# Optimization experiments

Measured on AMD Instinct MI355X. Metric: run time of the kernel, lower is better.

## Reference

```python
import jax, jax.numpy as jnp
import numpy as np

DEPTH = 8
DIM = 1024
DI = 2 * DIM        # d_inner (expand=2)
DSTATE = 16         # d_state
DCONV = 4           # conv kernel width
DTRANK = DIM // 16  # dt_rank = ceil(d_model/16) = 64
B = 2
L = 2048
EPS = 1e-5


def setup_inputs() -> dict:
    key = jax.random.key(0)
    ks = jax.random.split(key, 8)
    s = 0.02
    A_log = jnp.broadcast_to(
        jnp.log(jnp.arange(1, DSTATE + 1, dtype=jnp.float32)), (DEPTH, DI, DSTATE)
    )
    return {
        "x": jax.random.normal(ks[0], (B, L, DIM), jnp.float32),
        "in_proj_w": jax.random.normal(ks[1], (DEPTH, 2 * DI, DIM), jnp.float32) * s,
        "conv_w": jax.random.normal(ks[2], (DEPTH, DI, DCONV), jnp.float32) * s,
        "conv_b": jnp.zeros((DEPTH, DI), jnp.float32),
        "x_proj_w": jax.random.normal(ks[3], (DEPTH, DTRANK + 2 * DSTATE, DI), jnp.float32) * s,
        "dt_proj_w": jax.random.normal(ks[4], (DEPTH, DI, DTRANK), jnp.float32) * s,
        "dt_proj_b": jax.random.normal(ks[5], (DEPTH, DI), jnp.float32) * 0.1,
        "A_log": A_log + 0.0,
        "D": jnp.ones((DEPTH, DI), jnp.float32),
        "out_proj_w": jax.random.normal(ks[6], (DEPTH, DIM, DI), jnp.float32) * s,
        "rms_w": jnp.ones((DEPTH, DIM), jnp.float32),
    }


def _selective_scan(xs, delta, Bm, Cm, A):
    # xs, delta: [B, L, DI]; Bm, Cm: [B, L, DSTATE]; A: [DI, DSTATE]
    def step(h, t):
        dt, Bt, Ct, xt = t  # [B,DI], [B,N], [B,N], [B,DI]
        dA = jnp.exp(dt[:, :, None] * A)                      # [B,DI,N]
        h = dA * h + (dt * xt)[:, :, None] * Bt[:, None, :]   # [B,DI,N]
        y = jnp.einsum('bdn,bn->bd', h, Ct)                   # [B,DI]
        return h, y

    h0 = jnp.zeros((xs.shape[0], xs.shape[2], A.shape[1]), xs.dtype)
    ts = (delta.transpose(1, 0, 2), Bm.transpose(1, 0, 2),
          Cm.transpose(1, 0, 2), xs.transpose(1, 0, 2))
    _, ys = jax.lax.scan(step, h0, ts)  # ys: [L,B,DI]
    return ys.transpose(1, 0, 2)


def _mamba(x, Wi, cw, cb, Wx, Wdt, bdt, A_log, Dp, Wo):
    # in_proj (no bias): [B,L,DIM] -> [B,L,2*DI]
    xz = jnp.einsum('bld,ed->ble', x, Wi)
    xs, z = jnp.split(xz, 2, axis=-1)
    # depthwise causal conv1d, kernel DCONV, left pad DCONV-1
    xc = jax.lax.conv_general_dilated(
        xs.transpose(0, 2, 1), cw[:, None, :], (1,), [(DCONV - 1, 0)],
        dimension_numbers=('NCH', 'OIH', 'NCH'), feature_group_count=DI)
    xs = jax.nn.silu(xc + cb[None, :, None]).transpose(0, 2, 1)  # [B,L,DI]
    # x_proj -> dt, B, C
    xdbl = jnp.einsum('bld,ed->ble', xs, Wx)
    dt, Bm, Cm = jnp.split(xdbl, [DTRANK, DTRANK + DSTATE], axis=-1)
    delta = jax.nn.softplus(jnp.einsum('blr,dr->bld', dt, Wdt) + bdt)  # [B,L,DI]
    A = -jnp.exp(A_log)  # [DI, DSTATE]
    y = _selective_scan(xs, delta, Bm, Cm, A) + xs * Dp
    y = y * jax.nn.silu(z)
    return jnp.einsum('bld,ed->ble', y, Wo)  # out_proj, no bias


def _rmsnorm(x, w):
    return x * jax.lax.rsqrt(jnp.mean(x * x, axis=-1, keepdims=True) + EPS) * w


def reference(x, in_proj_w, conv_w, conv_b, x_proj_w, dt_proj_w, dt_proj_b,
              A_log, D, out_proj_w, rms_w):
    for i in range(DEPTH):
        x = _mamba(x, in_proj_w[i], conv_w[i], conv_b[i], x_proj_w[i],
                   dt_proj_w[i], dt_proj_b[i], A_log[i], D[i], out_proj_w[i])
        x = _rmsnorm(x, rms_w[i])
    return x
```

## Files before the change

kernel.cpp:

```cpp
#include <hip/hip_runtime.h>
#include <cstddef>

#define DEPTH  8
#define DIMM   1024
#define DI     2048
#define NST    16
#define DCONVK 4
#define DTRANK 64
#define BB     2
#define LL     2048
#define MM     (BB*LL)
#define BD     (BB*DI)
#define CHK    32
#define LC     (LL/CHK)
#define LOG2E  1.44269504088896f

typedef __attribute__((ext_vector_type(8))) short bf16x8;
typedef __attribute__((ext_vector_type(4))) float f32x4;

__device__ __forceinline__ unsigned short f2bf(float f) {
  unsigned int u = __float_as_uint(f);
  unsigned int r = (u + 0x7fffu + ((u >> 16) & 1u)) >> 16;
  return (unsigned short)r;
}
__device__ __forceinline__ float bf2f(unsigned short h) {
  return __uint_as_float(((unsigned int)h) << 16);
}

__global__ __launch_bounds__(256) void cvt2_k(const float* __restrict__ x,
                                              unsigned short* __restrict__ p,
                                              size_t n) {
  size_t i = ((size_t)blockIdx.x * 256 + threadIdx.x) * 4;
  float4 v = *(const float4*)(x + i);
  float vv[4] = {v.x, v.y, v.z, v.w};
  unsigned short u1[4], u2[4];
#pragma unroll
  for (int k = 0; k < 4; ++k) {
    unsigned short h1 = f2bf(vv[k]);
    u1[k] = h1;
    u2[k] = f2bf(vv[k] - bf2f(h1));
  }
  *(ushort4*)(p + i)     = make_ushort4(u1[0], u1[1], u1[2], u1[3]);
  *(ushort4*)(p + n + i) = make_ushort4(u2[0], u2[1], u2[2], u2[3]);
}

template <int BN, int NSPLIT>
__global__ __launch_bounds__(512, 2) void gemm2ph(
    const unsigned short* __restrict__ Ap, int lda_a, int pstr_a,
    const unsigned short* __restrict__ Bp, int lda_b, int pstr_b,
    float* __restrict__ C0, float* __restrict__ C1, int N, int Ktot) {
  constexpr int BM  = 256;
  constexpr int BF  = BN / 64;
  constexpr int BL  = BN / 128;
  constexpr int RA1 = BM * 32;
  constexpr int RB0 = 2 * BM * 32;
  constexpr int RB1 = 2 * BM * 32 + BN * 32;
  constexpr int BUFS = (2 * BM + 2 * BN) * 32;
  __shared__ unsigned short S[2 * BUFS];

  const int t  = threadIdx.x;
  const int w  = t >> 6;
  const int l  = t & 63;
  const int lm = l & 15;
  const int qs = ((l >> 4) << 3) ^ (((lm >> 1) & 3) << 3);

  const int nx   = gridDim.x;
  const int nwg  = nx * gridDim.y;
  const int flat = blockIdx.y * nx + blockIdx.x;
  const int swz  = (flat & 7) * (nwg >> 3) + (flat >> 3);
  const int m0 = (swz / nx) * BM;
  const int n0 = (swz % nx) * BN;
  const int z  = (NSPLIT == 2) ? blockIdx.z : 0;
  const int KS = Ktot / NSPLIT;

  const int wm = (w & 1) << 7;
  const int wn = (w >> 1) * (BN / 4);

  const int rr = t >> 2;
  const int kq = ((t & 3) ^ ((rr >> 1) & 3)) << 3;
  const unsigned short* srcA = Ap + (size_t)(m0 + rr) * lda_a + (size_t)z * KS + kq;
  const unsigned short* srcB = Bp + (size_t)(n0 + rr) * lda_b + (size_t)z * KS + kq;
  const size_t a128 = (size_t)128 * lda_a;
  const size_t b128 = (size_t)128 * lda_b;
  const int dbase = (w << 6) * 8;

#define GI(p_, off_)                                                           \
  __builtin_amdgcn_global_load_lds(                                            \
      (const __attribute__((address_space(1))) unsigned int*)(p_),             \
      (__attribute__((address_space(3))) unsigned int*)&S[bnext + (off_) + dbase], \
      16, 0, 0)

#define GI_PH0(kb_)                                                            \
  { GI(srcA + (kb_), 0); GI(srcA + a128 + (kb_), 4096);                        \
    GI(srcB + (kb_), RB0);                                                     \
    if (BL == 2) GI(srcB + b128 + (kb_), RB0 + 4096);                          \
    GI(srcB + (size_t)pstr_b + (kb_), RB1);                                    \
    if (BL == 2) GI(srcB + (size_t)pstr_b + b128 + (kb_), RB1 + 4096); }

#define GI_PH1(kb_)                                                            \
  { GI(srcA + (size_t)pstr_a + (kb_), RA1);                                    \
    GI(srcA + (size_t)pstr_a + a128 + (kb_), RA1 + 4096); }

  f32x4 acc[8][BF];
#pragma unroll
  for (int i = 0; i < 8; ++i)
#pragma unroll
    for (int j = 0; j < BF; ++j) acc[i][j] = (f32x4){0.f, 0.f, 0.f, 0.f};

  {
    const int bnext = 0;
    GI_PH0((size_t)0);
    GI_PH1((size_t)0);
  }
  asm volatile("s_waitcnt vmcnt(2)" ::: "memory");
  __builtin_amdgcn_s_barrier();

  const int NT = KS >> 5;
#pragma unroll 2
  for (int ti = 0; ti < NT; ++ti) {
    const int bcur  = (ti & 1) ? BUFS : 0;
    const int bnext = (ti & 1) ? 0 : BUFS;
    const size_t kb = (size_t)((ti + 1 < NT) ? (ti + 1) : 0) * 32;
    const unsigned short* Sb = &S[bcur];
    bf16x8 a[8], b0[BF], b1[BF];

#pragma unroll
    for (int i = 0; i < 8; ++i)
      a[i] = *(const bf16x8*)&Sb[(wm + i * 16 + lm) * 32 + qs];
#pragma unroll
    for (int j = 0; j < BF; ++j)
      b0[j] = *(const bf16x8*)&Sb[RB0 + (wn + j * 16 + lm) * 32 + qs];
#pragma unroll
    for (int j = 0; j < BF; ++j)
      b1[j] = *(const bf16x8*)&Sb[RB1 + (wn + j * 16 + lm) * 32 + qs];
    GI_PH0(kb);
    if constexpr (BN == 256) asm volatile("s_waitcnt vmcnt(6)" ::: "memory");
    else                     asm volatile("s_waitcnt vmcnt(4)" ::: "memory");
    __builtin_amdgcn_s_barrier();
    asm volatile("s_waitcnt lgkmcnt(0)" ::: "memory");
    __builtin_amdgcn_s_setprio(1);
#pragma unroll
    for (int i = 0; i < 8; ++i)
#pragma unroll
      for (int j = 0; j < BF; ++j)
        acc[i][j] = __builtin_amdgcn_mfma_f32_16x16x32_bf16(a[i], b0[j], acc[i][j], 0, 0, 0);
#pragma unroll
    for (int i = 0; i < 8; ++i)
#pragma unroll
      for (int j = 0; j < BF; ++j)
        acc[i][j] = __builtin_amdgcn_mfma_f32_16x16x32_bf16(a[i], b1[j], acc[i][j], 0, 0, 0);
    __builtin_amdgcn_s_setprio(0);
    __builtin_amdgcn_s_barrier();

#pragma unroll
    for (int i = 0; i < 8; ++i)
      a[i] = *(const bf16x8*)&Sb[RA1 + (wm + i * 16 + lm) * 32 + qs];
    GI_PH1(kb);
    asm volatile("s_waitcnt vmcnt(2)" ::: "memory");
    __builtin_amdgcn_s_barrier();
    asm volatile("s_waitcnt lgkmcnt(0)" ::: "memory");
    __builtin_amdgcn_s_setprio(1);
#pragma unroll
    for (int i = 0; i < 8; ++i)
#pragma unroll
      for (int j = 0; j < BF; ++j)
        acc[i][j] = __builtin_amdgcn_mfma_f32_16x16x32_bf16(a[i], b0[j], acc[i][j], 0, 0, 0);
    __builtin_amdgcn_s_setprio(0);
    __builtin_amdgcn_s_barrier();
  }
#undef GI_PH1
#undef GI_PH0
#undef GI

  float* Cc = (NSPLIT == 2 && blockIdx.z) ? C1 : C0;
  const int row0 = (l >> 4) << 2;
#pragma unroll
  for (int i = 0; i < 8; ++i)
#pragma unroll
    for (int j = 0; j < BF; ++j)
#pragma unroll
      for (int r = 0; r < 4; ++r) {
        int m = m0 + wm + i * 16 + row0 + r;
        int n = n0 + wn + j * 16 + lm;
        Cc[(size_t)m * N + n] = acc[i][j][r];
      }
}

__global__ __launch_bounds__(256) void dtproj_mp(const unsigned short* __restrict__ Ap,
                                                 const unsigned short* __restrict__ Bp,
                                                 const float* __restrict__ bdt,
                                                 float* __restrict__ Cd) {
  __shared__ unsigned short S[32768];
  const int t  = threadIdx.x;
  const int w  = t >> 6;
  const int l  = t & 63;
  const int lm = l & 15;
  const int q8 = (l >> 4) << 3;
  const int qs = q8 ^ (((lm >> 1) & 3) << 3);
  const int m0 = blockIdx.y * 128;
  const int n0 = blockIdx.x * 128;
  const int wm = (w & 1) << 6;
  const int wn = (w >> 1) << 6;

#pragma unroll
  for (int it = 0; it < 16; ++it) {
    int c  = it * 256 + t;
    int kt = c >> 11;
    int c2 = c & 2047;
    const unsigned short* base;
    int r, aslot;
    if (c2 < 1024) {
      int p = c2 >> 9; int wi = c2 & 511; r = wi >> 2; aslot = wi & 3;
      base = Ap + (size_t)p * (MM * 64) + (size_t)(m0 + r) * 64;
    } else {
      int c3 = c2 - 1024;
      int p = c3 >> 9; int wi = c3 & 511; r = wi >> 2; aslot = wi & 3;
      base = Bp + (size_t)p * (DI * 64) + (size_t)(n0 + r) * 64;
    }
    int kq = (aslot ^ ((r >> 1) & 3)) << 3;
    __builtin_amdgcn_global_load_lds(
        (const __attribute__((address_space(1))) unsigned int*)(base + kt * 32 + kq),
        (__attribute__((address_space(3))) unsigned int*)&S[(size_t)(it * 256 + (w << 6)) * 8],
        16, 0, 0);
  }
  __syncthreads();

  f32x4 acc[4][4];
#pragma unroll
  for (int i = 0; i < 4; ++i)
#pragma unroll
    for (int j = 0; j < 4; ++j) acc[i][j] = (f32x4){0.f, 0.f, 0.f, 0.f};

#pragma unroll
  for (int kt = 0; kt < 2; ++kt) {
    const int RA = kt * 16384;
    const int RB = kt * 16384 + 8192;
    bf16x8 a0[4], aX[4], b0[4];
#pragma unroll
    for (int i = 0; i < 4; ++i)
      a0[i] = *(const bf16x8*)&S[RA + (wm + i * 16 + lm) * 32 + qs];
#pragma unroll
    for (int j = 0; j < 4; ++j)
      b0[j] = *(const bf16x8*)&S[RB + (wn + j * 16 + lm) * 32 + qs];
#pragma unroll
    for (int i = 0; i < 4; ++i)
#pragma unroll
      for (int j = 0; j < 4; ++j)
        acc[i][j] = __builtin_amdgcn_mfma_f32_16x16x32_bf16(a0[i], b0[j], acc[i][j], 0, 0, 0);
#pragma unroll
    for (int j = 0; j < 4; ++j)
      aX[j] = *(const bf16x8*)&S[RB + 4096 + (wn + j * 16 + lm) * 32 + qs];
#pragma unroll
    for (int i = 0; i < 4; ++i)
#pragma unroll
      for (int j = 0; j < 4; ++j)
        acc[i][j] = __builtin_amdgcn_mfma_f32_16x16x32_bf16(a0[i], aX[j], acc[i][j], 0, 0, 0);
#pragma unroll
    for (int i = 0; i < 4; ++i)
      aX[i] = *(const bf16x8*)&S[RA + 4096 + (wm + i * 16 + lm) * 32 + qs];
#pragma unroll
    for (int i = 0; i < 4; ++i)
#pragma unroll
      for (int j = 0; j < 4; ++j)
        acc[i][j] = __builtin_amdgcn_mfma_f32_16x16x32_bf16(aX[i], b0[j], acc[i][j], 0, 0, 0);
  }

  const int row0 = (l >> 4) << 2;
#pragma unroll
  for (int j = 0; j < 4; ++j) {
    int n = n0 + wn + j * 16 + lm;
    float bv = bdt[n];
#pragma unroll
    for (int i = 0; i < 4; ++i)
#pragma unroll
      for (int r = 0; r < 4; ++r) {
        int m = m0 + wm + i * 16 + row0 + r;
        float x = acc[i][j][r] + bv;
        Cd[(size_t)m * DI + n] = fmaxf(x, 0.f) + log1pf(expf(-fabsf(x)));
      }
  }
}

#define XPN 96
__global__ __launch_bounds__(256) void xproj_part_k(const float* __restrict__ A,
                                                    const float* __restrict__ W,
                                                    float* __restrict__ Cp) {
  __shared__ float As[16][128];
  __shared__ float Ws[16][XPN];
  const int t  = threadIdx.x;
  const int tx = t & 15;
  const int ty = t >> 4;
  const int m0 = blockIdx.x * 128;
  const int kb = blockIdx.y * 256;
  float acc[8][6];
#pragma unroll
  for (int i = 0; i < 8; ++i)
#pragma unroll
    for (int j = 0; j < 6; ++j) acc[i][j] = 0.f;

  for (int k0 = kb; k0 < kb + 256; k0 += 16) {
#pragma unroll
    for (int e = t; e < 512; e += 256) {
      int r = e >> 2, cq = (e & 3) << 2;
      float4 v = *(const float4*)(A + (size_t)(m0 + r) * DI + k0 + cq);
      As[cq+0][r] = v.x; As[cq+1][r] = v.y; As[cq+2][r] = v.z; As[cq+3][r] = v.w;
    }
    for (int e = t; e < 384; e += 256) {
      int r = e >> 2, cq = (e & 3) << 2;
      float4 v = *(const float4*)(W + (size_t)r * DI + k0 + cq);
      Ws[cq+0][r] = v.x; Ws[cq+1][r] = v.y; Ws[cq+2][r] = v.z; Ws[cq+3][r] = v.w;
    }
    __syncthreads();
#pragma unroll
    for (int kk = 0; kk < 16; ++kk) {
      float a[8], b[6];
#pragma unroll
      for (int i = 0; i < 8; ++i) a[i] = As[kk][ty*8 + i];
#pragma unroll
      for (int j = 0; j < 6; ++j) b[j] = Ws[kk][tx*6 + j];
#pragma unroll
      for (int i = 0; i < 8; ++i)
#pragma unroll
        for (int j = 0; j < 6; ++j) acc[i][j] += a[i] * b[j];
    }
    __syncthreads();
  }
  float* cp = Cp + (size_t)blockIdx.y * MM * XPN;
#pragma unroll
  for (int i = 0; i < 8; ++i)
#pragma unroll
    for (int j = 0; j < 6; ++j)
      cp[(size_t)(m0 + ty*8 + i) * XPN + tx*6 + j] = acc[i][j];
}

__global__ __launch_bounds__(256) void xproj_red_k(const float* __restrict__ Cp,
                                                   float* __restrict__ o,
                                                   unsigned short* __restrict__ dtp) {
  int i = blockIdx.x * 256 + threadIdx.x;
  float s = 0.f;
#pragma unroll
  for (int ks = 0; ks < 8; ++ks) s += Cp[(size_t)ks * (MM * XPN) + i];
  o[i] = s;
  int m = i / 96, col = i - m * 96;
  if (col < DTRANK) {
    unsigned short h1 = f2bf(s);
    dtp[(size_t)m * DTRANK + col] = h1;
    dtp[(size_t)MM * DTRANK + (size_t)m * DTRANK + col] = f2bf(s - bf2f(h1));
  }
}

__device__ __forceinline__ float fast_silu(float x) {
  return x * __builtin_amdgcn_rcpf(1.f + exp2f(-LOG2E * x));
}

__global__ __launch_bounds__(256) void conv_silu_k(const float* __restrict__ xz,
                                                   const float* __restrict__ cw,
                                                   const float* __restrict__ cb,
                                                   float* __restrict__ xc) {
  int idx = blockIdx.x * 256 + threadIdx.x;
  int c  = idx & (DI - 1);
  int bl = idx >> 11;
  int l  = bl & (LL - 1);
  float acc = cb[c];
#pragma unroll
  for (int k = 0; k < DCONVK; ++k) {
    int ls = l - (DCONVK - 1) + k;
    if (ls >= 0)
      acc += xz[(size_t)(bl - (DCONVK - 1) + k) * (2*DI) + c] * cw[c*DCONVK + k];
  }
  xc[idx] = fast_silu(acc);
}

__global__ __launch_bounds__(256) void scan_pass1(const float* __restrict__ delta,
                                                  const float* __restrict__ xc,
                                                  const float* __restrict__ xdbl,
                                                  const float* __restrict__ A_log,
                                                  float* __restrict__ Hc,
                                                  float* __restrict__ Sdt) {
  const int t  = threadIdx.x;
  const int c  = blockIdx.x >> 6;
  const int g  = blockIdx.x & 63;
  const int q  = t >> 2;
  const int nq = t & 3;
  const int ch = g * 64 + q;
  const int b  = ch >> 11;
  const int d  = ch & (DI - 1);
  const size_t rowbase = (size_t)b * LL + (size_t)c * LC;

  __shared__ float Bs[LC * 16];
  { int row = t >> 2, seg = t & 3;
    *(float4*)&Bs[row * 16 + seg * 4] =
        *(const float4*)(xdbl + (rowbase + row) * 96 + DTRANK + seg * 4);
  }
  __syncthreads();

  float4 al = *(const float4*)(A_log + (size_t)d * NST + nq * 4);
  const float Av0 = -expf(al.x) * LOG2E, Av1 = -expf(al.y) * LOG2E;
  const float Av2_ = -expf(al.z) * LOG2E, Av3 = -expf(al.w) * LOG2E;
  float h0 = 0.f, h1 = 0.f, h2 = 0.f, h3 = 0.f, S = 0.f;

#define P1_SU 4
  float aD[P1_SU], aX[P1_SU];
  float bD[P1_SU], bX[P1_SU];

#define P1_LOAD(l0, D_, X_)                                            \
  { _Pragma("unroll")                                                  \
    for (int u = 0; u < P1_SU; ++u) {                                  \
      size_t bl = rowbase + (l0) + u;                                  \
      D_[u] = delta[bl * DI + d];                                      \
      X_[u] = xc[bl * DI + d];                                         \
    } }

#define P1_COMP(l0, D_, X_)                                            \
  { _Pragma("unroll")                                                  \
    for (int u = 0; u < P1_SU; ++u) {                                  \
      float4 Bv = *(const float4*)&Bs[((l0) + u) * 16 + nq * 4];       \
      float dt = D_[u], uB = dt * X_[u];                               \
      h0 = fmaf(exp2f(dt * Av0), h0, uB * Bv.x);                       \
      h1 = fmaf(exp2f(dt * Av1), h1, uB * Bv.y);                       \
      h2 = fmaf(exp2f(dt * Av2_), h2, uB * Bv.z);                      \
      h3 = fmaf(exp2f(dt * Av3), h3, uB * Bv.w);                       \
      S += dt;                                                         \
    } }

  P1_LOAD(0, aD, aX);
  for (int l0 = 0; l0 < LC; l0 += 2 * P1_SU) {
    P1_LOAD(l0 + P1_SU, bD, bX);
    P1_COMP(l0, aD, aX);
    if (l0 + 2 * P1_SU < LC) P1_LOAD(l0 + 2 * P1_SU, aD, aX);
    P1_COMP(l0 + P1_SU, bD, bX);
  }
#undef P1_LOAD
#undef P1_COMP
  size_t hi = ((size_t)c * BD + ch) * NST + nq * 4;
  float4 hv; hv.x = h0; hv.y = h1; hv.z = h2; hv.w = h3;
  *(float4*)(Hc + hi) = hv;
  if (nq == 0) Sdt[(size_t)c * BD + ch] = S;
}

__global__ __launch_bounds__(256) void scan_pass2(float* __restrict__ Hc,
                                                  const float* __restrict__ Sdt,
                                                  const float* __restrict__ A_log) {
  const int g  = blockIdx.x * 256 + threadIdx.x;
  const int n  = g & (NST - 1);
  const int ch = g >> 4;
  const int d  = ch & (DI - 1);
  const float Av2 = -expf(A_log[d * NST + n]) * LOG2E;
  float Sv[CHK];
#pragma unroll
  for (int c = 0; c < CHK; ++c) Sv[c] = Sdt[(size_t)c * BD + ch];
  float h = 0.f;
  float tmp = Hc[(size_t)ch * NST + n];
#pragma unroll
  for (int c = 0; c < CHK; ++c) {
    size_t idx = ((size_t)c * BD + ch) * NST + n;
    float tnext = (c + 1 < CHK) ? Hc[((size_t)(c+1) * BD + ch) * NST + n] : 0.f;
    Hc[idx] = h;
    h = fmaf(exp2f(Av2 * Sv[c]), h, tmp);
    tmp = tnext;
  }
}

__global__ __launch_bounds__(256) void scan_pass3(const float* __restrict__ delta,
                                                  const float* __restrict__ xc,
                                                  const float* __restrict__ xdbl,
                                                  const float* __restrict__ A_log,
                                                  float* __restrict__ xzp,
                                                  const float* __restrict__ Dp,
                                                  const float* __restrict__ Hc) {
  const int t  = threadIdx.x;
  const int c  = blockIdx.x >> 6;
  const int g  = blockIdx.x & 63;
  const int q  = t >> 2;
  const int nq = t & 3;
  const int ch = g * 64 + q;
  const int b  = ch >> 11;
  const int d  = ch & (DI - 1);
  const size_t rowbase = (size_t)b * LL + (size_t)c * LC;

  __shared__ float BCs[LC * 32];
  {
#pragma unroll
    for (int e = t; e < 512; e += 256) {
      int row = e >> 3, seg = e & 7;
      *(float4*)&BCs[row * 32 + seg * 4] =
          *(const float4*)(xdbl + (rowbase + row) * 96 + DTRANK + seg * 4);
    }
  }
  __syncthreads();

  float4 al = *(const float4*)(A_log + (size_t)d * NST + nq * 4);
  const float Av0 = -expf(al.x) * LOG2E, Av1 = -expf(al.y) * LOG2E;
  const float Av2_ = -expf(al.z) * LOG2E, Av3 = -expf(al.w) * LOG2E;
  const float Dv = Dp[d];
  float4 hv = *(const float4*)(Hc + ((size_t)c * BD + ch) * NST + nq * 4);
  float h0 = hv.x, h1 = hv.y, h2 = hv.z, h3 = hv.w;
  unsigned short* yp = (unsigned short*)xzp;

#define P3_SU 2
  float aD[P3_SU], aX[P3_SU], aZ[P3_SU];
  float bD[P3_SU], bX[P3_SU], bZ[P3_SU];

#define P3_LOAD(l0, D_, X_, Z_)                                        \
  { _Pragma("unroll")                                                  \
    for (int u = 0; u < P3_SU; ++u) {                                  \
      size_t bl = rowbase + (l0) + u;                                  \
      D_[u] = delta[bl * DI + d];                                      \
      X_[u] = xc[bl * DI + d];                                         \
      Z_[u] = xzp[bl * (2*DI) + DI + d];                               \
    } }

#define P3_COMP(l0, D_, X_, Z_)                                        \
  { _Pragma("unroll")                                                  \
    for (int u = 0; u < P3_SU; ++u) {                                  \
      float4 Bv = *(const float4*)&BCs[((l0) + u) * 32 + nq * 4];      \
      float4 Cv = *(const float4*)&BCs[((l0) + u) * 32 + 16 + nq * 4]; \
      float dt = D_[u], uB = dt * X_[u];                               \
      h0 = fmaf(exp2f(dt * Av0), h0, uB * Bv.x);                       \
      h1 = fmaf(exp2f(dt * Av1), h1, uB * Bv.y);                       \
      h2 = fmaf(exp2f(dt * Av2_), h2, uB * Bv.z);                      \
      h3 = fmaf(exp2f(dt * Av3), h3, uB * Bv.w);                       \
      float s = fmaf(h1, Cv.y, h0 * Cv.x);                             \
      float t2 = fmaf(h3, Cv.w, h2 * Cv.z);                            \
      s += t2;                                                         \
      s += __shfl_xor(s, 1, 4);                                        \
      s += __shfl_xor(s, 2, 4);                                        \
      if (nq == 0) {                                                   \
        float yv = (s + X_[u] * Dv) * fast_silu(Z_[u]);                \
        unsigned short y1 = f2bf(yv);                                  \
        unsigned short y2 = f2bf(yv - bf2f(y1));                       \
        size_t bl = rowbase + (l0) + u;                                \
        yp[bl * 8192 + d] = y1;                                        \
        yp[bl * 8192 + 2048 + d] = y2;                                 \
      }                                                                \
    } }

  P3_LOAD(0, aD, aX, aZ);
  for (int l0 = 0; l0 < LC; l0 += 2 * P3_SU) {
    P3_LOAD(l0 + P3_SU, bD, bX, bZ);
    P3_COMP(l0, aD, aX, aZ);
    if (l0 + 2 * P3_SU < LC) P3_LOAD(l0 + 2 * P3_SU, aD, aX, aZ);
    P3_COMP(l0 + P3_SU, bD, bX, bZ);
  }
#undef P3_LOAD
#undef P3_COMP
}

template <bool PLANES>
__global__ __launch_bounds__(256) void rmsnorm_k(const float* __restrict__ x,
                                                 const float* __restrict__ x2,
                                                 const float* __restrict__ w,
                                                 float* __restrict__ o,
                                                 unsigned short* __restrict__ op) {
  int row = blockIdx.x;
  const float* xr  = x  + (size_t)row * DIMM;
  const float* x2r = x2 + (size_t)row * DIMM;
  float s = 0.f;
  for (int i = threadIdx.x; i < DIMM; i += 256) {
    float v = xr[i] + x2r[i]; s += v * v;
  }
#pragma unroll
  for (int off = 32; off > 0; off >>= 1) s += __shfl_xor(s, off, 64);
  __shared__ float red[4];
  if ((threadIdx.x & 63) == 0) red[threadIdx.x >> 6] = s;
  __syncthreads();
  float tot = red[0] + red[1] + red[2] + red[3];
  float scale = rsqrtf(tot * (1.0f / DIMM) + 1e-5f);
  for (int i = threadIdx.x; i < DIMM; i += 256) {
    float v = (xr[i] + x2r[i]) * scale * w[i];
    if (PLANES) {
      unsigned short h1 = f2bf(v);
      op[(size_t)row * DIMM + i] = h1;
      op[(size_t)MM * DIMM + (size_t)row * DIMM + i] = f2bf(v - bf2f(h1));
    } else {
      o[(size_t)row * DIMM + i] = v;
    }
  }
}

extern "C" void kernel_launch(void* const* d_in, const int* in_sizes, int n_in,
                              void* d_out, int out_size, void* d_ws, size_t ws_size,
                              hipStream_t stream) {
  (void)in_sizes; (void)n_in; (void)out_size; (void)ws_size;
  const float* x_in    = (const float*)d_in[0];
  const float* Wi_all  = (const float*)d_in[1];
  const float* cw_all  = (const float*)d_in[2];
  const float* cb_all  = (const float*)d_in[3];
  const float* Wx_all  = (const float*)d_in[4];
  const float* Wdt_all = (const float*)d_in[5];
  const float* bdt_all = (const float*)d_in[6];
  const float* Alog_all= (const float*)d_in[7];
  const float* D_all   = (const float*)d_in[8];
  const float* Wo_all  = (const float*)d_in[9];
  const float* rw_all  = (const float*)d_in[10];
  float* out = (float*)d_out;

  float* ws    = (float*)d_ws;
  float* xz    = ws;
  float* xc    = xz   + (size_t)MM * 2 * DI;
  float* xdbl  = xc   + (size_t)MM * DI;
  float* delta = xdbl + (size_t)MM * 96;
  float* xbuf  = delta+ (size_t)MM * DI;
  float* outtmp = xc;

  unsigned short* xpl  = (unsigned short*)delta;
  unsigned short* wipl = (unsigned short*)xc;
  unsigned short* wopl = (unsigned short*)(xc + (size_t)4194304);
  float*          Cp   = delta;
  float* part1 = delta + (size_t)4194304;
  float* Hc   = xbuf;
  float* Sdt  = Hc + (size_t)CHK * BD * NST;
  unsigned short* dtpl  = (unsigned short*)(xbuf + 2228224);
  unsigned short* wdtpl = (unsigned short*)(xbuf + 2490368);

  const int EW_GRID = (MM * DI) / 256;
  const int SCAN_GRID = CHK * 64;

  for (int i = 0; i < DEPTH; ++i) {
    const float* Wi   = Wi_all  + (size_t)i * (2*DI) * DIMM;
    const float* cw   = cw_all  + (size_t)i * DI * DCONVK;
    const float* cb   = cb_all  + (size_t)i * DI;
    const float* Wx   = Wx_all  + (size_t)i * 96 * DI;
    const float* Wdt  = Wdt_all + (size_t)i * DI * DTRANK;
    const float* bdt  = bdt_all + (size_t)i * DI;
    const float* Alog = Alog_all+ (size_t)i * DI * NST;
    const float* Dp   = D_all   + (size_t)i * DI;
    const float* Wo   = Wo_all  + (size_t)i * DIMM * DI;
    const float* rw   = rw_all  + (size_t)i * DIMM;

    if (i == 0)
      cvt2_k<<<(MM*DIMM)/1024, 256, 0, stream>>>(x_in, xpl, (size_t)MM * DIMM);
    cvt2_k<<<((2*DI)*DIMM)/1024, 256, 0, stream>>>(Wi, wipl, (size_t)(2*DI) * DIMM);
    gemm2ph<256,1><<<dim3((2*DI)/256, MM/256, 1), 512, 0, stream>>>(
        xpl, DIMM, MM*DIMM, wipl, DIMM, (2*DI)*DIMM, xz, nullptr, 2*DI, DIMM);
    conv_silu_k<<<EW_GRID, 256, 0, stream>>>(xz, cw, cb, xc);
    xproj_part_k<<<dim3(MM/128, 8), 256, 0, stream>>>(xc, Wx, Cp);
    xproj_red_k<<<(MM*XPN)/256, 256, 0, stream>>>(Cp, xdbl, dtpl);
    cvt2_k<<<(DI*DTRANK)/1024, 256, 0, stream>>>(Wdt, wdtpl, (size_t)DI * DTRANK);
    dtproj_mp<<<dim3(DI/128, MM/128), 256, 0, stream>>>(dtpl, wdtpl, bdt, delta);
    scan_pass1<<<SCAN_GRID, 256, 0, stream>>>(delta, xc, xdbl, Alog, Hc, Sdt);
    scan_pass2<<<(BD*NST)/256, 256, 0, stream>>>(Hc, Sdt, Alog);
    scan_pass3<<<SCAN_GRID, 256, 0, stream>>>(delta, xc, xdbl, Alog, xz, Dp, Hc);
    cvt2_k<<<(DIMM*DI)/1024, 256, 0, stream>>>(Wo, wopl, (size_t)DIMM * DI);
    gemm2ph<128,2><<<dim3(DIMM/128, MM/256, 2), 512, 0, stream>>>(
        (const unsigned short*)xz, 8192, 2048, wopl, DI, DIMM*DI,
        outtmp, part1, DIMM, DI);
    if (i < DEPTH - 1)
      rmsnorm_k<true><<<MM, 256, 0, stream>>>(outtmp, part1, rw, nullptr, xpl);
    else
      rmsnorm_k<false><<<MM, 256, 0, stream>>>(outtmp, part1, rw, out, nullptr);
  }
}
```

Measured before the change: 3.259 ms.

## Split GEMM K-step into three load phases and stage scan tiles in LDS

The split-precision GEMM now issues the B-low plane load as its own phase. Each K-step runs three MFMA phases (a0·b0, a0·b1, a1·b0), so the global-to-LDS copies interleave more finely with compute, and the vmcnt waits are adjusted to match. The scan pass1 and pass3 kernels now load delta, xc and z tiles into shared memory with coalesced float4 loads instead of strided per-thread scalar loads. Pass3 also buffers the bf16 output planes in LDS and writes them back vectorised. This adds barriers and LDS use, which may lower occupancy, and relies on correct vmcnt counts.

```diff
diff --git a/kernel.cpp b/kernel.cpp
--- a/kernel.cpp
+++ b/kernel.cpp
@@ -45,7 +45,7 @@
 }
 
 template <int BN, int NSPLIT>
-__global__ __launch_bounds__(512, 2) void gemm2ph(
+__global__ __launch_bounds__(512, 2) void gemm3ph(
     const unsigned short* __restrict__ Ap, int lda_a, int pstr_a,
     const unsigned short* __restrict__ Bp, int lda_b, int pstr_b,
     float* __restrict__ C0, float* __restrict__ C1, int N, int Ktot) {
@@ -54,7 +54,7 @@
   constexpr int BL  = BN / 128;
   constexpr int RA1 = BM * 32;
   constexpr int RB0 = 2 * BM * 32;
-  constexpr int RB1 = 2 * BM * 32 + BN * 32;
+  constexpr int RB1 = RB0 + BN * 32;
   constexpr int BUFS = (2 * BM + 2 * BN) * 32;
   __shared__ unsigned short S[2 * BUFS];
 
@@ -93,11 +93,13 @@
 #define GI_PH0(kb_)                                                            \
   { GI(srcA + (kb_), 0); GI(srcA + a128 + (kb_), 4096);                        \
     GI(srcB + (kb_), RB0);                                                     \
-    if (BL == 2) GI(srcB + b128 + (kb_), RB0 + 4096);                          \
-    GI(srcB + (size_t)pstr_b + (kb_), RB1);                                    \
-    if (BL == 2) GI(srcB + (size_t)pstr_b + b128 + (kb_), RB1 + 4096); }
+    if constexpr (BL == 2) GI(srcB + b128 + (kb_), RB0 + 4096); }
 
 #define GI_PH1(kb_)                                                            \
+  { GI(srcB + (size_t)pstr_b + (kb_), RB1);                                    \
+    if constexpr (BL == 2) GI(srcB + (size_t)pstr_b + b128 + (kb_), RB1 + 4096); }
+
+#define GI_PH2(kb_)                                                            \
   { GI(srcA + (size_t)pstr_a + (kb_), RA1);                                    \
     GI(srcA + (size_t)pstr_a + a128 + (kb_), RA1 + 4096); }
 
@@ -111,8 +113,10 @@
     const int bnext = 0;
     GI_PH0((size_t)0);
     GI_PH1((size_t)0);
-  }
-  asm volatile("s_waitcnt vmcnt(2)" ::: "memory");
+    GI_PH2((size_t)0);
+  }
+  if constexpr (BN == 256) asm volatile("s_waitcnt vmcnt(4)" ::: "memory");
+  else                     asm volatile("s_waitcnt vmcnt(3)" ::: "memory");
   __builtin_amdgcn_s_barrier();
 
   const int NT = KS >> 5;
@@ -130,10 +134,24 @@
 #pragma unroll
     for (int j = 0; j < BF; ++j)
       b0[j] = *(const bf16x8*)&Sb[RB0 + (wn + j * 16 + lm) * 32 + qs];
+    GI_PH0(kb);
+    if constexpr (BN == 256) asm volatile("s_waitcnt vmcnt(6)" ::: "memory");
+    else                     asm volatile("s_waitcnt vmcnt(5)" ::: "memory");
+    __builtin_amdgcn_s_barrier();
+    asm volatile("s_waitcnt lgkmcnt(0)" ::: "memory");
+    __builtin_amdgcn_s_setprio(1);
+#pragma unroll
+    for (int i = 0; i < 8; ++i)
+#pragma unroll
+      for (int j = 0; j < BF; ++j)
+        acc[i][j] = __builtin_amdgcn_mfma_f32_16x16x32_bf16(a[i], b0[j], acc[i][j], 0, 0, 0);
+    __builtin_amdgcn_s_setprio(0);
+    __builtin_amdgcn_s_barrier();
+
 #pragma unroll
     for (int j = 0; j < BF; ++j)
       b1[j] = *(const bf16x8*)&Sb[RB1 + (wn + j * 16 + lm) * 32 + qs];
-    GI_PH0(kb);
+    GI_PH1(kb);
     if constexpr (BN == 256) asm volatile("s_waitcnt vmcnt(6)" ::: "memory");
     else                     asm volatile("s_waitcnt vmcnt(4)" ::: "memory");
     __builtin_amdgcn_s_barrier();
@@ -143,11 +161,6 @@
     for (int i = 0; i < 8; ++i)
 #pragma unroll
       for (int j = 0; j < BF; ++j)
-        acc[i][j] = __builtin_amdgcn_mfma_f32_16x16x32_bf16(a[i], b0[j], acc[i][j], 0, 0, 0);
-#pragma unroll
-    for (int i = 0; i < 8; ++i)
-#pragma unroll
-      for (int j = 0; j < BF; ++j)
         acc[i][j] = __builtin_amdgcn_mfma_f32_16x16x32_bf16(a[i], b1[j], acc[i][j], 0, 0, 0);
     __builtin_amdgcn_s_setprio(0);
     __builtin_amdgcn_s_barrier();
@@ -155,8 +168,9 @@
 #pragma unroll
     for (int i = 0; i < 8; ++i)
       a[i] = *(const bf16x8*)&Sb[RA1 + (wm + i * 16 + lm) * 32 + qs];
-    GI_PH1(kb);
-    asm volatile("s_waitcnt vmcnt(2)" ::: "memory");
+    GI_PH2(kb);
+    if constexpr (BN == 256) asm volatile("s_waitcnt vmcnt(4)" ::: "memory");
+    else                     asm volatile("s_waitcnt vmcnt(3)" ::: "memory");
     __builtin_amdgcn_s_barrier();
     asm volatile("s_waitcnt lgkmcnt(0)" ::: "memory");
     __builtin_amdgcn_s_setprio(1);
@@ -168,6 +182,7 @@
     __builtin_amdgcn_s_setprio(0);
     __builtin_amdgcn_s_barrier();
   }
+#undef GI_PH2
 #undef GI_PH1
 #undef GI_PH0
 #undef GI
@@ -385,12 +400,22 @@
   const int ch = g * 64 + q;
   const int b  = ch >> 11;
   const int d  = ch & (DI - 1);
+  const int dbs = (g & 31) * 64;
   const size_t rowbase = (size_t)b * LL + (size_t)c * LC;
 
   __shared__ float Bs[LC * 16];
+  __shared__ float Ds[LC][64];
+  __shared__ float Xs[LC][64];
   { int row = t >> 2, seg = t & 3;
     *(float4*)&Bs[row * 16 + seg * 4] =
         *(const float4*)(xdbl + (rowbase + row) * 96 + DTRANK + seg * 4);
+  }
+#pragma unroll
+  for (int e = t; e < LC * 16; e += 256) {
+    int row = e >> 4, seg = (e & 15) << 2;
+    size_t ga = (rowbase + row) * DI + dbs + seg;
+    *(float4*)&Ds[row][seg] = *(const float4*)(delta + ga);
+    *(float4*)&Xs[row][seg] = *(const float4*)(xc + ga);
   }
   __syncthreads();
 
@@ -399,39 +424,18 @@
   const float Av2_ = -expf(al.z) * LOG2E, Av3 = -expf(al.w) * LOG2E;
   float h0 = 0.f, h1 = 0.f, h2 = 0.f, h3 = 0.f, S = 0.f;
 
-#define P1_SU 4
-  float aD[P1_SU], aX[P1_SU];
-  float bD[P1_SU], bX[P1_SU];
-
-#define P1_LOAD(l0, D_, X_)                                            \
-  { _Pragma("unroll")                                                  \
-    for (int u = 0; u < P1_SU; ++u) {                                  \
-      size_t bl = rowbase + (l0) + u;                                  \
-      D_[u] = delta[bl * DI + d];                                      \
-      X_[u] = xc[bl * DI + d];                                         \
-    } }
-
-#define P1_COMP(l0, D_, X_)                                            \
-  { _Pragma("unroll")                                                  \
-    for (int u = 0; u < P1_SU; ++u) {                                  \
-      float4 Bv = *(const float4*)&Bs[((l0) + u) * 16 + nq * 4];       \
-      float dt = D_[u], uB = dt * X_[u];                               \
-      h0 = fmaf(exp2f(dt * Av0), h0, uB * Bv.x);                       \
-      h1 = fmaf(exp2f(dt * Av1), h1, uB * Bv.y);                       \
-      h2 = fmaf(exp2f(dt * Av2_), h2, uB * Bv.z);                      \
-      h3 = fmaf(exp2f(dt * Av3), h3, uB * Bv.w);                       \
-      S += dt;                                                         \
-    } }
-
-  P1_LOAD(0, aD, aX);
-  for (int l0 = 0; l0 < LC; l0 += 2 * P1_SU) {
-    P1_LOAD(l0 + P1_SU, bD, bX);
-    P1_COMP(l0, aD, aX);
-    if (l0 + 2 * P1_SU < LC) P1_LOAD(l0 + 2 * P1_SU, aD, aX);
-    P1_COMP(l0 + P1_SU, bD, bX);
-  }
-#undef P1_LOAD
-#undef P1_COMP
+#pragma unroll 4
+  for (int l = 0; l < LC; ++l) {
+    float dt = Ds[l][q];
+    float xv = Xs[l][q];
+    float4 Bv = *(const float4*)&Bs[l * 16 + nq * 4];
+    float uB = dt * xv;
+    h0 = fmaf(exp2f(dt * Av0), h0, uB * Bv.x);
+    h1 = fmaf(exp2f(dt * Av1), h1, uB * Bv.y);
+    h2 = fmaf(exp2f(dt * Av2_), h2, uB * Bv.z);
+    h3 = fmaf(exp2f(dt * Av3), h3, uB * Bv.w);
+    S += dt;
+  }
   size_t hi = ((size_t)c * BD + ch) * NST + nq * 4;
   float4 hv; hv.x = h0; hv.y = h1; hv.z = h2; hv.w = h3;
   *(float4*)(Hc + hi) = hv;
@@ -476,16 +480,29 @@
   const int ch = g * 64 + q;
   const int b  = ch >> 11;
   const int d  = ch & (DI - 1);
+  const int dbs = (g & 31) * 64;
   const size_t rowbase = (size_t)b * LL + (size_t)c * LC;
 
   __shared__ float BCs[LC * 32];
-  {
-#pragma unroll
-    for (int e = t; e < 512; e += 256) {
-      int row = e >> 3, seg = e & 7;
-      *(float4*)&BCs[row * 32 + seg * 4] =
-          *(const float4*)(xdbl + (rowbase + row) * 96 + DTRANK + seg * 4);
-    }
+  __shared__ float Ds[LC][64];
+  __shared__ float Xs[LC][64];
+  __shared__ float Zs[LC][64];
+  __shared__ unsigned short Y1s[LC][64];
+  __shared__ unsigned short Y2s[LC][64];
+#pragma unroll
+  for (int e = t; e < 512; e += 256) {
+    int row = e >> 3, seg = e & 7;
+    *(float4*)&BCs[row * 32 + seg * 4] =
+        *(const float4*)(xdbl + (rowbase + row) * 96 + DTRANK + seg * 4);
+  }
+#pragma unroll
+  for (int e = t; e < LC * 16; e += 256) {
+    int row = e >> 4, seg = (e & 15) << 2;
+    size_t ga = (rowbase + row) * DI + dbs + seg;
+    *(float4*)&Ds[row][seg] = *(const float4*)(delta + ga);
+    *(float4*)&Xs[row][seg] = *(const float4*)(xc + ga);
+    *(float4*)&Zs[row][seg] =
+        *(const float4*)(xzp + (rowbase + row) * (2*DI) + DI + dbs + seg);
   }
   __syncthreads();
 
@@ -495,55 +512,40 @@
   const float Dv = Dp[d];
   float4 hv = *(const float4*)(Hc + ((size_t)c * BD + ch) * NST + nq * 4);
   float h0 = hv.x, h1 = hv.y, h2 = hv.z, h3 = hv.w;
+
+#pragma unroll 2
+  for (int l = 0; l < LC; ++l) {
+    float dt = Ds[l][q];
+    float xv = Xs[l][q];
+    float4 Bv = *(const float4*)&BCs[l * 32 + nq * 4];
+    float4 Cv = *(const float4*)&BCs[l * 32 + 16 + nq * 4];
+    float uB = dt * xv;
+    h0 = fmaf(exp2f(dt * Av0), h0, uB * Bv.x);
+    h1 = fmaf(exp2f(dt * Av1), h1, uB * Bv.y);
+    h2 = fmaf(exp2f(dt * Av2_), h2, uB * Bv.z);
+    h3 = fmaf(exp2f(dt * Av3), h3, uB * Bv.w);
+    float s = fmaf(h1, Cv.y, h0 * Cv.x);
+    float t2 = fmaf(h3, Cv.w, h2 * Cv.z);
+    s += t2;
+    s += __shfl_xor(s, 1, 4);
+    s += __shfl_xor(s, 2, 4);
+    if (nq == 0) {
+      float yv = (s + xv * Dv) * fast_silu(Zs[l][q]);
+      unsigned short y1 = f2bf(yv);
+      Y1s[l][q] = y1;
+      Y2s[l][q] = f2bf(yv - bf2f(y1));
+    }
+  }
+  __syncthreads();
+
   unsigned short* yp = (unsigned short*)xzp;
-
-#define P3_SU 2
-  float aD[P3_SU], aX[P3_SU], aZ[P3_SU];
-  float bD[P3_SU], bX[P3_SU], bZ[P3_SU];
-
-#define P3_LOAD(l0, D_, X_, Z_)                                        \
-  { _Pragma("unroll")                                                  \
-    for (int u = 0; u < P3_SU; ++u) {                                  \
-      size_t bl = rowbase + (l0) + u;                                  \
-      D_[u] = delta[bl * DI + d];                                      \
-      X_[u] = xc[bl * DI + d];                                         \
-      Z_[u] = xzp[bl * (2*DI) + DI + d];                               \
-    } }
-
-#define P3_COMP(l0, D_, X_, Z_)                                        \
-  { _Pragma("unroll")                                                  \
-    for (int u = 0; u < P3_SU; ++u) {                                  \
-      float4 Bv = *(const float4*)&BCs[((l0) + u) * 32 + nq * 4];      \
-      float4 Cv = *(const float4*)&BCs[((l0) + u) * 32 + 16 + nq * 4]; \
-      float dt = D_[u], uB = dt * X_[u];                               \
-      h0 = fmaf(exp2f(dt * Av0), h0, uB * Bv.x);                       \
-      h1 = fmaf(exp2f(dt * Av1), h1, uB * Bv.y);                       \
-      h2 = fmaf(exp2f(dt * Av2_), h2, uB * Bv.z);                      \
-      h3 = fmaf(exp2f(dt * Av3), h3, uB * Bv.w);                       \
-      float s = fmaf(h1, Cv.y, h0 * Cv.x);                             \
-      float t2 = fmaf(h3, Cv.w, h2 * Cv.z);                            \
-      s += t2;                                                         \
-      s += __shfl_xor(s, 1, 4);                                        \
-      s += __shfl_xor(s, 2, 4);                                        \
-      if (nq == 0) {                                                   \
-        float yv = (s + X_[u] * Dv) * fast_silu(Z_[u]);                \
-        unsigned short y1 = f2bf(yv);                                  \
-        unsigned short y2 = f2bf(yv - bf2f(y1));                       \
-        size_t bl = rowbase + (l0) + u;                                \
-        yp[bl * 8192 + d] = y1;                                        \
-        yp[bl * 8192 + 2048 + d] = y2;                                 \
-      }                                                                \
-    } }
-
-  P3_LOAD(0, aD, aX, aZ);
-  for (int l0 = 0; l0 < LC; l0 += 2 * P3_SU) {
-    P3_LOAD(l0 + P3_SU, bD, bX, bZ);
-    P3_COMP(l0, aD, aX, aZ);
-    if (l0 + 2 * P3_SU < LC) P3_LOAD(l0 + 2 * P3_SU, aD, aX, aZ);
-    P3_COMP(l0 + P3_SU, bD, bX, bZ);
-  }
-#undef P3_LOAD
-#undef P3_COMP
+#pragma unroll
+  for (int e = t; e < LC * 16; e += 256) {
+    int row = e >> 4, seg = (e & 15) << 2;
+    size_t base = (rowbase + row) * 8192 + dbs + seg;
+    *(ushort4*)(yp + base)        = *(const ushort4*)&Y1s[row][seg];
+    *(ushort4*)(yp + base + 2048) = *(const ushort4*)&Y2s[row][seg];
+  }
 }
 
 template <bool PLANES>
@@ -631,7 +633,7 @@
     if (i == 0)
       cvt2_k<<<(MM*DIMM)/1024, 256, 0, stream>>>(x_in, xpl, (size_t)MM * DIMM);
     cvt2_k<<<((2*DI)*DIMM)/1024, 256, 0, stream>>>(Wi, wipl, (size_t)(2*DI) * DIMM);
-    gemm2ph<256,1><<<dim3((2*DI)/256, MM/256, 1), 512, 0, stream>>>(
+    gemm3ph<256,1><<<dim3((2*DI)/256, MM/256, 1), 512, 0, stream>>>(
         xpl, DIMM, MM*DIMM, wipl, DIMM, (2*DI)*DIMM, xz, nullptr, 2*DI, DIMM);
     conv_silu_k<<<EW_GRID, 256, 0, stream>>>(xz, cw, cb, xc);
     xproj_part_k<<<dim3(MM/128, 8), 256, 0, stream>>>(xc, Wx, Cp);
@@ -642,7 +644,7 @@
     scan_pass2<<<(BD*NST)/256, 256, 0, stream>>>(Hc, Sdt, Alog);
     scan_pass3<<<SCAN_GRID, 256, 0, stream>>>(delta, xc, xdbl, Alog, xz, Dp, Hc);
     cvt2_k<<<(DIMM*DI)/1024, 256, 0, stream>>>(Wo, wopl, (size_t)DIMM * DI);
-    gemm2ph<128,2><<<dim3(DIMM/128, MM/256, 2), 512, 0, stream>>>(
+    gemm3ph<128,2><<<dim3(DIMM/128, MM/256, 2), 512, 0, stream>>>(
         (const unsigned short*)xz, 8192, 2048, wopl, DI, DIMM*DI,
         outtmp, part1, DIMM, DI);
     if (i < DEPTH - 1)
```

Result: slower. 3.541 ms (+8.7%).

## Split split-bf16 GEMM loop into three phases and stage scan outputs in LDS

Applied to the files above, without the earlier changes.

The two-plane bf16 GEMM main loop now runs three phases instead of two. The B-low-plane load gets its own phase and barrier, so the first MFMA batch can start as soon as the A-high and B-high tiles arrive, with finer-grained overlap of global-to-LDS loads and compute. Separately, the scan output kernel buffers its y high/low bf16 values in shared memory and writes them out with coalesced ushort4 stores, replacing scattered 2-byte stores per channel. The cost is one more barrier per GEMM k-step, extra LDS in the scan kernel, and wait counts that must stay consistent with the load counts per phase.

```diff
diff --git a/kernel.cpp b/kernel.cpp
--- a/kernel.cpp
+++ b/kernel.cpp
@@ -45,7 +45,7 @@
 }
 
 template <int BN, int NSPLIT>
-__global__ __launch_bounds__(512, 2) void gemm2ph(
+__global__ __launch_bounds__(512, 2) void gemm3ph(
     const unsigned short* __restrict__ Ap, int lda_a, int pstr_a,
     const unsigned short* __restrict__ Bp, int lda_b, int pstr_b,
     float* __restrict__ C0, float* __restrict__ C1, int N, int Ktot) {
@@ -54,7 +54,7 @@
   constexpr int BL  = BN / 128;
   constexpr int RA1 = BM * 32;
   constexpr int RB0 = 2 * BM * 32;
-  constexpr int RB1 = 2 * BM * 32 + BN * 32;
+  constexpr int RB1 = RB0 + BN * 32;
   constexpr int BUFS = (2 * BM + 2 * BN) * 32;
   __shared__ unsigned short S[2 * BUFS];
 
@@ -93,11 +93,13 @@
 #define GI_PH0(kb_)                                                            \
   { GI(srcA + (kb_), 0); GI(srcA + a128 + (kb_), 4096);                        \
     GI(srcB + (kb_), RB0);                                                     \
-    if (BL == 2) GI(srcB + b128 + (kb_), RB0 + 4096);                          \
-    GI(srcB + (size_t)pstr_b + (kb_), RB1);                                    \
-    if (BL == 2) GI(srcB + (size_t)pstr_b + b128 + (kb_), RB1 + 4096); }
+    if constexpr (BL == 2) GI(srcB + b128 + (kb_), RB0 + 4096); }
 
 #define GI_PH1(kb_)                                                            \
+  { GI(srcB + (size_t)pstr_b + (kb_), RB1);                                    \
+    if constexpr (BL == 2) GI(srcB + (size_t)pstr_b + b128 + (kb_), RB1 + 4096); }
+
+#define GI_PH2(kb_)                                                            \
   { GI(srcA + (size_t)pstr_a + (kb_), RA1);                                    \
     GI(srcA + (size_t)pstr_a + a128 + (kb_), RA1 + 4096); }
 
@@ -111,8 +113,10 @@
     const int bnext = 0;
     GI_PH0((size_t)0);
     GI_PH1((size_t)0);
-  }
-  asm volatile("s_waitcnt vmcnt(2)" ::: "memory");
+    GI_PH2((size_t)0);
+  }
+  if constexpr (BN == 256) asm volatile("s_waitcnt vmcnt(4)" ::: "memory");
+  else                     asm volatile("s_waitcnt vmcnt(3)" ::: "memory");
   __builtin_amdgcn_s_barrier();
 
   const int NT = KS >> 5;
@@ -130,10 +134,24 @@
 #pragma unroll
     for (int j = 0; j < BF; ++j)
       b0[j] = *(const bf16x8*)&Sb[RB0 + (wn + j * 16 + lm) * 32 + qs];
+    GI_PH0(kb);
+    if constexpr (BN == 256) asm volatile("s_waitcnt vmcnt(6)" ::: "memory");
+    else                     asm volatile("s_waitcnt vmcnt(5)" ::: "memory");
+    __builtin_amdgcn_s_barrier();
+    asm volatile("s_waitcnt lgkmcnt(0)" ::: "memory");
+    __builtin_amdgcn_s_setprio(1);
+#pragma unroll
+    for (int i = 0; i < 8; ++i)
+#pragma unroll
+      for (int j = 0; j < BF; ++j)
+        acc[i][j] = __builtin_amdgcn_mfma_f32_16x16x32_bf16(a[i], b0[j], acc[i][j], 0, 0, 0);
+    __builtin_amdgcn_s_setprio(0);
+    __builtin_amdgcn_s_barrier();
+
 #pragma unroll
     for (int j = 0; j < BF; ++j)
       b1[j] = *(const bf16x8*)&Sb[RB1 + (wn + j * 16 + lm) * 32 + qs];
-    GI_PH0(kb);
+    GI_PH1(kb);
     if constexpr (BN == 256) asm volatile("s_waitcnt vmcnt(6)" ::: "memory");
     else                     asm volatile("s_waitcnt vmcnt(4)" ::: "memory");
     __builtin_amdgcn_s_barrier();
@@ -143,11 +161,6 @@
     for (int i = 0; i < 8; ++i)
 #pragma unroll
       for (int j = 0; j < BF; ++j)
-        acc[i][j] = __builtin_amdgcn_mfma_f32_16x16x32_bf16(a[i], b0[j], acc[i][j], 0, 0, 0);
-#pragma unroll
-    for (int i = 0; i < 8; ++i)
-#pragma unroll
-      for (int j = 0; j < BF; ++j)
         acc[i][j] = __builtin_amdgcn_mfma_f32_16x16x32_bf16(a[i], b1[j], acc[i][j], 0, 0, 0);
     __builtin_amdgcn_s_setprio(0);
     __builtin_amdgcn_s_barrier();
@@ -155,8 +168,9 @@
 #pragma unroll
     for (int i = 0; i < 8; ++i)
       a[i] = *(const bf16x8*)&Sb[RA1 + (wm + i * 16 + lm) * 32 + qs];
-    GI_PH1(kb);
-    asm volatile("s_waitcnt vmcnt(2)" ::: "memory");
+    GI_PH2(kb);
+    if constexpr (BN == 256) asm volatile("s_waitcnt vmcnt(4)" ::: "memory");
+    else                     asm volatile("s_waitcnt vmcnt(3)" ::: "memory");
     __builtin_amdgcn_s_barrier();
     asm volatile("s_waitcnt lgkmcnt(0)" ::: "memory");
     __builtin_amdgcn_s_setprio(1);
@@ -168,6 +182,7 @@
     __builtin_amdgcn_s_setprio(0);
     __builtin_amdgcn_s_barrier();
   }
+#undef GI_PH2
 #undef GI_PH1
 #undef GI_PH0
 #undef GI
@@ -476,9 +491,12 @@
   const int ch = g * 64 + q;
   const int b  = ch >> 11;
   const int d  = ch & (DI - 1);
+  const int dbs = (g & 31) * 64;
   const size_t rowbase = (size_t)b * LL + (size_t)c * LC;
 
   __shared__ float BCs[LC * 32];
+  __shared__ unsigned short Y1s[LC][64];
+  __shared__ unsigned short Y2s[LC][64];
   {
 #pragma unroll
     for (int e = t; e < 512; e += 256) {
@@ -495,7 +513,6 @@
   const float Dv = Dp[d];
   float4 hv = *(const float4*)(Hc + ((size_t)c * BD + ch) * NST + nq * 4);
   float h0 = hv.x, h1 = hv.y, h2 = hv.z, h3 = hv.w;
-  unsigned short* yp = (unsigned short*)xzp;
 
 #define P3_SU 2
   float aD[P3_SU], aX[P3_SU], aZ[P3_SU];
@@ -528,10 +545,8 @@
       if (nq == 0) {                                                   \
         float yv = (s + X_[u] * Dv) * fast_silu(Z_[u]);                \
         unsigned short y1 = f2bf(yv);                                  \
-        unsigned short y2 = f2bf(yv - bf2f(y1));                       \
-        size_t bl = rowbase + (l0) + u;                                \
-        yp[bl * 8192 + d] = y1;                                        \
-        yp[bl * 8192 + 2048 + d] = y2;                                 \
+        Y1s[(l0) + u][q] = y1;                                         \
+        Y2s[(l0) + u][q] = f2bf(yv - bf2f(y1));                        \
       }                                                                \
     } }
 
@@ -544,6 +559,16 @@
   }
 #undef P3_LOAD
 #undef P3_COMP
+  __syncthreads();
+
+  unsigned short* yp = (unsigned short*)xzp;
+#pragma unroll
+  for (int e = t; e < LC * 16; e += 256) {
+    int row = e >> 4, seg = (e & 15) << 2;
+    size_t base = (rowbase + row) * 8192 + dbs + seg;
+    *(ushort4*)(yp + base)        = *(const ushort4*)&Y1s[row][seg];
+    *(ushort4*)(yp + base + 2048) = *(const ushort4*)&Y2s[row][seg];
+  }
 }
 
 template <bool PLANES>
@@ -631,7 +656,7 @@
     if (i == 0)
       cvt2_k<<<(MM*DIMM)/1024, 256, 0, stream>>>(x_in, xpl, (size_t)MM * DIMM);
     cvt2_k<<<((2*DI)*DIMM)/1024, 256, 0, stream>>>(Wi, wipl, (size_t)(2*DI) * DIMM);
-    gemm2ph<256,1><<<dim3((2*DI)/256, MM/256, 1), 512, 0, stream>>>(
+    gemm3ph<256,1><<<dim3((2*DI)/256, MM/256, 1), 512, 0, stream>>>(
         xpl, DIMM, MM*DIMM, wipl, DIMM, (2*DI)*DIMM, xz, nullptr, 2*DI, DIMM);
     conv_silu_k<<<EW_GRID, 256, 0, stream>>>(xz, cw, cb, xc);
     xproj_part_k<<<dim3(MM/128, 8), 256, 0, stream>>>(xc, Wx, Cp);
@@ -642,7 +667,7 @@
     scan_pass2<<<(BD*NST)/256, 256, 0, stream>>>(Hc, Sdt, Alog);
     scan_pass3<<<SCAN_GRID, 256, 0, stream>>>(delta, xc, xdbl, Alog, xz, Dp, Hc);
     cvt2_k<<<(DIMM*DI)/1024, 256, 0, stream>>>(Wo, wopl, (size_t)DIMM * DI);
-    gemm2ph<128,2><<<dim3(DIMM/128, MM/256, 2), 512, 0, stream>>>(
+    gemm3ph<128,2><<<dim3(DIMM/128, MM/256, 2), 512, 0, stream>>>(
         (const unsigned short*)xz, 8192, 2048, wopl, DI, DIMM*DI,
         outtmp, part1, DIMM, DI);
     if (i < DEPTH - 1)
```

After: 3.222 ms. No clear change (-1.1%).
